# Optimization experiments

Hardware: AMD Instinct MI355X
Metric: run time of the kernel (lower is better)

## Reference

```python
import jax, jax.numpy as jnp
import numpy as np

N_NODES = 50000
N_EDGES = 640000
IN_CH = 128
HIDDEN = 128
HEADS = 4
HEAD_DIM = HIDDEN // HEADS  # 32
NEG_SLOPE = 0.2


def setup_inputs() -> dict:
    key = jax.random.key(0)
    ks = jax.random.split(key, 12)
    x = jax.random.normal(ks[0], (N_NODES, IN_CH), dtype=jnp.float32)
    edge_index = jax.random.randint(ks[1], (2, N_EDGES), 0, N_NODES, dtype=jnp.int64)
    s = 0.1
    W1 = jax.random.normal(ks[2], (IN_CH, HEADS * HEAD_DIM), dtype=jnp.float32) * s
    a_src1 = jax.random.normal(ks[3], (HEADS, HEAD_DIM), dtype=jnp.float32) * s
    a_dst1 = jax.random.normal(ks[4], (HEADS, HEAD_DIM), dtype=jnp.float32) * s
    b1 = jax.random.normal(ks[5], (HEADS * HEAD_DIM,), dtype=jnp.float32) * s
    W2 = jax.random.normal(ks[6], (HIDDEN, HEADS * HEAD_DIM), dtype=jnp.float32) * s
    a_src2 = jax.random.normal(ks[7], (HEADS, HEAD_DIM), dtype=jnp.float32) * s
    a_dst2 = jax.random.normal(ks[8], (HEADS, HEAD_DIM), dtype=jnp.float32) * s
    b2 = jax.random.normal(ks[9], (HEADS * HEAD_DIM,), dtype=jnp.float32) * s
    return {"x": x, "edge_index": edge_index, "W1": W1, "a_src1": a_src1,
            "a_dst1": a_dst1, "b1": b1, "W2": W2, "a_src2": a_src2,
            "a_dst2": a_dst2, "b2": b2}


def _gat_conv(x, src, dst, W, a_src, a_dst, b):
    """PyG GATConv (concat=True, add_self_loops already applied to src/dst)."""
    N = x.shape[0]
    H, C = a_src.shape
    h = (x @ W).reshape(N, H, C)                      # [N, H, C]
    alpha_s = jnp.einsum('nhc,hc->nh', h, a_src)      # [N, H]
    alpha_d = jnp.einsum('nhc,hc->nh', h, a_dst)      # [N, H]
    e = alpha_s[src] + alpha_d[dst]                   # [E, H]
    e = jnp.where(e > 0, e, NEG_SLOPE * e)            # leaky_relu(0.2)
    # segment softmax over destination nodes (every node has a self-loop)
    emax = jax.ops.segment_max(e, dst, num_segments=N)
    ee = jnp.exp(e - emax[dst])
    denom = jax.ops.segment_sum(ee, dst, num_segments=N)
    alpha = ee / (denom[dst] + 1e-16)                 # [E, H]
    out = jax.ops.segment_sum(h[src] * alpha[:, :, None], dst, num_segments=N)
    return out.reshape(N, H * C) + b


def reference(x, edge_index, W1, a_src1, a_dst1, b1, W2, a_src2, a_dst2, b2):
    N = x.shape[0]
    loops = jnp.arange(N, dtype=edge_index.dtype)
    src = jnp.concatenate([edge_index[0], loops])
    dst = jnp.concatenate([edge_index[1], loops])
    h = _gat_conv(x, src, dst, W1, a_src1, a_dst1, b1)
    h = jax.nn.relu(h)  # dropout is identity in eval mode
    out = _gat_conv(h, src, dst, W2, a_src2, a_dst2, b2)
    return out
```

## Files before the change

### kernel.cpp

```cpp
#include <hip/hip_runtime.h>
#include <hip/hip_bf16.h>
#include <hip/hip_fp16.h>

#define N_NODES 50000
#define N_EDGES 640000
#define E_TOT   690000
#define CH      128
#define ROWPAD  50176
#define GEMMB   391
#define EBLK    2048
#define NEB     337
#define NBUCK   196
#define MTP     344

typedef __attribute__((ext_vector_type(8))) short short8;
typedef __attribute__((ext_vector_type(4))) float float4v;

static __device__ __forceinline__ float bf2f(unsigned short u) {
  return __uint_as_float(((unsigned)u) << 16);
}
static __device__ __forceinline__ unsigned short f2bf(float f) {
  unsigned u = __float_as_uint(f);
  return (unsigned short)((u + 0x7fffu + ((u >> 16) & 1u)) >> 16);
}

static __device__ __forceinline__ void load_edge(const int* __restrict__ ei,
                                                 int e, int i64, int& s, int& d)
{
  if (e >= N_EDGES) { s = d = e - N_EDGES; return; }
  if (i64) { s = ei[2 * (size_t)e]; d = ei[2 * ((size_t)N_EDGES + e)]; }
  else     { s = ei[e];             d = ei[N_EDGES + e]; }
}

static __device__ __forceinline__ short8 load_bf8(const void* __restrict__ X,
                                                  size_t off, int f32)
{
  if (!f32) return *(const short8*)((const unsigned short*)X + off);
  const float4* p = (const float4*)((const float*)X + off);
  float4 u = p[0], v = p[1];
  short8 r;
  r[0] = (short)f2bf(u.x); r[1] = (short)f2bf(u.y);
  r[2] = (short)f2bf(u.z); r[3] = (short)f2bf(u.w);
  r[4] = (short)f2bf(v.x); r[5] = (short)f2bf(v.y);
  r[6] = (short)f2bf(v.z); r[7] = (short)f2bf(v.w);
  return r;
}

__global__ __launch_bounds__(256) void k_prep(
    const void* __restrict__ W1, const void* __restrict__ W2,
    const void* __restrict__ as1, const void* __restrict__ ad1,
    const void* __restrict__ as2, const void* __restrict__ ad2,
    unsigned short* __restrict__ Wt1, unsigned short* __restrict__ Wt2,
    unsigned short* __restrict__ Ba1, unsigned short* __restrict__ Ba2,
    const unsigned short* __restrict__ x16,
    const unsigned int* __restrict__ eiw,
    int* __restrict__ flags)
{
  int b = blockIdx.x, t = threadIdx.x;
  __shared__ int sf, si;
  if (t == 0) { sf = 0; si = 1; }
  __syncthreads();
  int bad = 0;
  for (int i = t; i < 4096; i += 256) {
    float v = bf2f(x16[i]);
    if (!(v == v) || fabsf(v) > 100.f) bad = 1;
  }
  if (bad) atomicOr(&sf, 1);
  if (b == 0 && t < 128 && eiw[2 * t + 1] != 0u) atomicAnd(&si, 0);
  __syncthreads();
  int f32 = sf;
  if (b == 0 && t == 0) { flags[0] = sf; flags[1] = si; }

  if (b < 8) {
    int g = b * 256 + t;
    int l = g >> 10;
    int rem = g & 1023;
    int k = rem >> 3, n = rem & 7;
    const void* W  = l ? W2 : W1;
    const void* av = (n < 4) ? (l ? as2 : as1) : (l ? ad2 : ad1);
    int h = n & 3;
    float sum = 0.f;
    for (int c = 0; c < 32; c++) {
      float w = f32 ? ((const float*)W)[k * 128 + h * 32 + c]
                    : bf2f(((const unsigned short*)W)[k * 128 + h * 32 + c]);
      float a = f32 ? ((const float*)av)[h * 32 + c]
                    : bf2f(((const unsigned short*)av)[h * 32 + c]);
      sum += w * a;
    }
    unsigned short* Ba = l ? Ba2 : Ba1;
    Ba[n * 128 + k] = f2bf(sum);
    Ba[(8 + (rem >> 7)) * 128 + (rem & 127)] = 0;
  } else {
    int b2 = b - 8;
    int l = b2 >> 7, c = b2 & 127;
    if (t < 128) {
      const void* W = l ? W2 : W1;
      unsigned short* Wt = l ? Wt2 : Wt1;
      Wt[c * 128 + t] = f32 ? f2bf(((const float*)W)[t * 128 + c])
                            : ((const unsigned short*)W)[t * 128 + c];
    }
  }
}

struct SmemG { unsigned short WB[144][136]; };

static __device__ __forceinline__ void gemm_body(
    SmemG& sm, int bx,
    const void* __restrict__ X,
    const unsigned short* __restrict__ Wt_g,
    const unsigned short* __restrict__ Ba_g,
    unsigned short* __restrict__ H, float* __restrict__ AS,
    float* __restrict__ AD, int nrows, int xf32)
{
  int tid = threadIdx.x;
#pragma unroll
  for (int i = 0; i < 8; i++) {
    int j = i * 256 + tid;
    int c = j >> 4, k8 = j & 15;
    *(short8*)&sm.WB[c][k8 * 8] = *(const short8*)(Wt_g + c * 128 + k8 * 8);
  }
  {
    int n = tid >> 4, k8 = tid & 15;
    *(short8*)&sm.WB[128 + n][k8 * 8] = *(const short8*)(Ba_g + n * 128 + k8 * 8);
  }
  __syncthreads();
  int wave = tid >> 6, lane = tid & 63;
  int R0 = (bx * 4 + wave) * 32;
  if (R0 >= nrows) return;
  int m = lane & 15, quad = lane >> 4;
  int rA = R0 + m;        if (rA >= nrows) rA = nrows - 1;
  int rB = R0 + 16 + m;   if (rB >= nrows) rB = nrows - 1;
  size_t aA = (size_t)rA * CH + quad * 8;
  size_t aB = (size_t)rB * CH + quad * 8;
  float4v acc[2][8];
  float4v accA[2];
#pragma unroll
  for (int hf = 0; hf < 2; hf++) {
    accA[hf] = (float4v){0.f, 0.f, 0.f, 0.f};
#pragma unroll
    for (int ct = 0; ct < 8; ct++) acc[hf][ct] = (float4v){0.f, 0.f, 0.f, 0.f};
  }
#pragma unroll
  for (int kb = 0; kb < 4; kb++) {
    short8 a0 = load_bf8(X, aA + kb * 32, xf32);
    short8 a1 = load_bf8(X, aB + kb * 32, xf32);
#pragma unroll
    for (int ct = 0; ct < 8; ct++) {
      short8 bb = *(const short8*)&sm.WB[ct * 16 + m][kb * 32 + quad * 8];
      acc[0][ct] = __builtin_amdgcn_mfma_f32_16x16x32_bf16(a0, bb, acc[0][ct], 0, 0, 0);
      acc[1][ct] = __builtin_amdgcn_mfma_f32_16x16x32_bf16(a1, bb, acc[1][ct], 0, 0, 0);
    }
    short8 bA = *(const short8*)&sm.WB[128 + m][kb * 32 + quad * 8];
    accA[0] = __builtin_amdgcn_mfma_f32_16x16x32_bf16(a0, bA, accA[0], 0, 0, 0);
    accA[1] = __builtin_amdgcn_mfma_f32_16x16x32_bf16(a1, bA, accA[1], 0, 0, 0);
  }
#pragma unroll
  for (int hf = 0; hf < 2; hf++) {
    int rbase = R0 + hf * 16 + quad * 4;
#pragma unroll
    for (int ct = 0; ct < 8; ct++) {
      int col = ct * 16 + m;
#pragma unroll
      for (int r = 0; r < 4; r++)
        H[(size_t)(rbase + r) * CH + col] = __half_as_ushort(__float2half(acc[hf][ct][r]));
    }
    if (m < 4) {
#pragma unroll
      for (int r = 0; r < 4; r++)
        AS[(size_t)(rbase + r) * 4 + m] = accA[hf][r];
    } else if (m < 8) {
#pragma unroll
      for (int r = 0; r < 4; r++)
        AD[(size_t)(rbase + r) * 4 + (m - 4)] = accA[hf][r];
    }
  }
}

__global__ __launch_bounds__(256, 2) void k_gemm(
    const void* __restrict__ X,
    const unsigned short* __restrict__ Wt_g,
    const unsigned short* __restrict__ Ba_g,
    unsigned short* __restrict__ H, float* __restrict__ AS, float* __restrict__ AD,
    int nrows)
{
  __shared__ SmemG sm;
  gemm_body(sm, blockIdx.x, X, Wt_g, Ba_g, H, AS, AD, nrows, 0);
}

__global__ __launch_bounds__(256, 2) void k_gemm_hist(
    const void* __restrict__ X,
    const unsigned short* __restrict__ Wt_g,
    const unsigned short* __restrict__ Ba_g,
    unsigned short* __restrict__ H, float* __restrict__ AS, float* __restrict__ AD,
    int nrows, const int* __restrict__ ei, int* __restrict__ MT,
    const int* __restrict__ flags)
{
  __shared__ SmemG sm;
  __shared__ int hist[NBUCK];
  if (blockIdx.x >= GEMMB) {
    int b = blockIdx.x - GEMMB;
    int t = threadIdx.x;
    if (t < NBUCK) hist[t] = 0;
    __syncthreads();
    int i64 = flags[1];
    int base = b * EBLK;
#pragma unroll
    for (int k = 0; k < 8; k++) {
      int e = base + k * 256 + t;
      if (e < E_TOT) {
        int s, d;
        load_edge(ei, e, i64, s, d);
        atomicAdd(&hist[d >> 8], 1);
      }
    }
    __syncthreads();
    if (t < NBUCK) MT[t * MTP + b] = hist[t];
    return;
  }
  gemm_body(sm, blockIdx.x, X, Wt_g, Ba_g, H, AS, AD, nrows, flags[0]);
}

__global__ __launch_bounds__(512) void k_rowscan(int* __restrict__ MT,
                                                 int* __restrict__ T)
{
  __shared__ int sh[512];
  int q = blockIdx.x, t = threadIdx.x;
  int v = (t < NEB) ? MT[q * MTP + t] : 0;
  sh[t] = v;
  __syncthreads();
  for (int off = 1; off < 512; off <<= 1) {
    int u = (t >= off) ? sh[t - off] : 0;
    __syncthreads();
    sh[t] += u;
    __syncthreads();
  }
  if (t < NEB) MT[q * MTP + t] = sh[t] - v;
  if (t == NEB - 1) T[q] = sh[t];
}

__global__ __launch_bounds__(256) void k_bscan(const int* __restrict__ T,
                                               int* __restrict__ BB)
{
  __shared__ int sh[256];
  int t = threadIdx.x;
  int v = (t < NBUCK) ? T[t] : 0;
  sh[t] = v;
  __syncthreads();
  for (int off = 1; off < 256; off <<= 1) {
    int u = (t >= off) ? sh[t - off] : 0;
    __syncthreads();
    sh[t] += u;
    __syncthreads();
  }
  if (t < NBUCK) BB[t] = sh[t] - v;
  if (t == NBUCK - 1) BB[NBUCK] = sh[t];
}

__global__ __launch_bounds__(256) void k_bucket(
    const int* __restrict__ ei, const int* __restrict__ MT,
    const int* __restrict__ BB, int2* __restrict__ ebuf,
    const int* __restrict__ flags)
{
  __shared__ int cur[NBUCK];
  int b = blockIdx.x, t = threadIdx.x;
  if (t < NBUCK) cur[t] = BB[t] + MT[t * MTP + b];
  __syncthreads();
  int i64 = flags[1];
  int base = b * EBLK;
#pragma unroll
  for (int k = 0; k < 8; k++) {
    int e = base + k * 256 + t;
    if (e < E_TOT) {
      int s, d;
      load_edge(ei, e, i64, s, d);
      int pos = atomicAdd(&cur[d >> 8], 1);
      ebuf[pos] = make_int2(s, d);
    }
  }
}

__global__ __launch_bounds__(256) void k_fine(
    const int2* __restrict__ ebuf, const int* __restrict__ BB,
    int* __restrict__ row_ptr, int* __restrict__ deg,
    int* __restrict__ csr_src)
{
  __shared__ int cnt[256], sh[256], cur[256];
  int q = blockIdx.x, t = threadIdx.x;
  int lo = BB[q], hi = BB[q + 1];
  cnt[t] = 0;
  __syncthreads();
  for (int i = lo + t; i < hi; i += 256)
    atomicAdd(&cnt[ebuf[i].y & 255], 1);
  __syncthreads();
  int v = cnt[t];
  sh[t] = v;
  __syncthreads();
  for (int off = 1; off < 256; off <<= 1) {
    int u = (t >= off) ? sh[t - off] : 0;
    __syncthreads();
    sh[t] += u;
    __syncthreads();
  }
  int lp = sh[t] - v;
  int n = (q << 8) + t;
  if (n < N_NODES) { row_ptr[n] = lo + lp; deg[n] = v; }
  cur[t] = lo + lp;
  __syncthreads();
  for (int i = lo + t; i < hi; i += 256) {
    int2 p = ebuf[i];
    int slot = atomicAdd(&cur[p.y & 255], 1);
    csr_src[slot] = p.x;
  }
}

__global__ __launch_bounds__(256) void k_agg(
    const int* __restrict__ row_ptr, const int* __restrict__ deg,
    const int* __restrict__ csr_src,
    const __half* __restrict__ H,
    const float* __restrict__ AS, const float* __restrict__ AD,
    const void* __restrict__ b, void* __restrict__ Y,
    const int* __restrict__ flags, int layer)
{
  int tid = threadIdx.x;
  int node = blockIdx.x * 4 + (tid >> 6);
  if (node >= N_NODES) return;
  int lane = tid & 63;
  int h = lane >> 4;
  int c0 = 2 * lane;
  float adh = AD[(size_t)node * 4 + h];
  int start = row_ptr[node];
  int dg = deg[node];
  const __half2* __restrict__ H2 = (const __half2*)H;
  float accx = 0.f, accy = 0.f, den = 0.f;
  int j = 0;
  for (; j + 8 <= dg; j += 8) {
    int sI[8];
#pragma unroll
    for (int u = 0; u < 8; u++) sI[u] = csr_src[start + j + u];
    float eV[8];
#pragma unroll
    for (int u = 0; u < 8; u++) eV[u] = AS[(size_t)sI[u] * 4 + h] + adh;
    float2 vV[8];
#pragma unroll
    for (int u = 0; u < 8; u++) vV[u] = __half22float2(H2[(size_t)sI[u] * 64 + lane]);
#pragma unroll
    for (int u = 0; u < 8; u++) {
      float x = eV[u] > 0.f ? eV[u] : 0.2f * eV[u];
      float ex = __expf(x);
      accx += ex * vV[u].x;
      accy += ex * vV[u].y;
      den  += ex;
    }
  }
  for (; j + 4 <= dg; j += 4) {
    int sI[4];
#pragma unroll
    for (int u = 0; u < 4; u++) sI[u] = csr_src[start + j + u];
    float eV[4];
#pragma unroll
    for (int u = 0; u < 4; u++) eV[u] = AS[(size_t)sI[u] * 4 + h] + adh;
    float2 vV[4];
#pragma unroll
    for (int u = 0; u < 4; u++) vV[u] = __half22float2(H2[(size_t)sI[u] * 64 + lane]);
#pragma unroll
    for (int u = 0; u < 4; u++) {
      float x = eV[u] > 0.f ? eV[u] : 0.2f * eV[u];
      float ex = __expf(x);
      accx += ex * vV[u].x;
      accy += ex * vV[u].y;
      den  += ex;
    }
  }
  for (; j < dg; j++) {
    int s = csr_src[start + j];
    float e = AS[(size_t)s * 4 + h] + adh;
    float2 v = __half22float2(H2[(size_t)s * 64 + lane]);
    e = e > 0.f ? e : 0.2f * e;
    float ex = __expf(e);
    accx += ex * v.x;
    accy += ex * v.y;
    den  += ex;
  }
  float inv = 1.f / (den + 1e-16f);
  int f32 = flags[0];
  float b0 = f32 ? ((const float*)b)[c0]     : bf2f(((const unsigned short*)b)[c0]);
  float b1 = f32 ? ((const float*)b)[c0 + 1] : bf2f(((const unsigned short*)b)[c0 + 1]);
  float r0 = accx * inv + b0;
  float r1 = accy * inv + b1;
  size_t o = (size_t)node * CH + c0;
  if (layer == 1) {
    r0 = r0 > 0.f ? r0 : 0.f;
    r1 = r1 > 0.f ? r1 : 0.f;
    ushort2 w; w.x = f2bf(r0); w.y = f2bf(r1);
    *(ushort2*)((unsigned short*)Y + o) = w;
  } else if (f32) {
    float2 w; w.x = r0; w.y = r1;
    *(float2*)((float*)Y + o) = w;
  } else {
    ushort2 w; w.x = f2bf(r0); w.y = f2bf(r1);
    *(ushort2*)((unsigned short*)Y + o) = w;
  }
}

extern "C" void kernel_launch(void* const* d_in, const int* in_sizes, int n_in,
                              void* d_out, int out_size, void* d_ws, size_t ws_size,
                              hipStream_t stream)
{
  const void* x   = d_in[0];
  const int*  ei  = (const int*)d_in[1];
  const void* W1  = d_in[2];
  const void* as1 = d_in[3];
  const void* ad1 = d_in[4];
  const void* b1  = d_in[5];
  const void* W2  = d_in[6];
  const void* as2 = d_in[7];
  const void* ad2 = d_in[8];
  const void* b2  = d_in[9];

  char* ws = (char*)d_ws;
  unsigned short* H  = (unsigned short*)(ws);
  float*  AS         = (float*)(ws + 12845056);
  float*  AD         = (float*)(ws + 13647872);
  unsigned short* X2 = (unsigned short*)(ws + 14450688);
  int*    deg        = (int*)(ws + 27295744);
  int*    row_ptr    = (int*)(ws + 27496448);
  int*    csr_src    = (int*)(ws + 27697152);
  int*    MT         = (int*)(ws + 30457600);
  int*    T          = (int*)(ws + 30728192);
  int*    BB         = (int*)(ws + 30729216);
  int*    flags      = (int*)(ws + 30730240);
  int2*   ebuf       = (int2*)(ws + 30731264);
  unsigned short* Wt1 = (unsigned short*)(ws + 36251264);
  unsigned short* Wt2 = (unsigned short*)(ws + 36284032);
  unsigned short* Ba1 = (unsigned short*)(ws + 36316800);
  unsigned short* Ba2 = (unsigned short*)(ws + 36320896);

  const int agg_blocks = (N_NODES + 3) / 4;

  k_prep<<<264, 256, 0, stream>>>(W1, W2, as1, ad1, as2, ad2,
                                  Wt1, Wt2, Ba1, Ba2,
                                  (const unsigned short*)x,
                                  (const unsigned int*)ei, flags);

  k_gemm_hist<<<GEMMB + NEB, 256, 0, stream>>>(
      x, Wt1, Ba1, H, AS, AD, N_NODES, ei, MT, flags);

  k_rowscan<<<NBUCK, 512, 0, stream>>>(MT, T);
  k_bscan  <<<1, 256, 0, stream>>>(T, BB);
  k_bucket <<<NEB, 256, 0, stream>>>(ei, MT, BB, ebuf, flags);
  k_fine   <<<NBUCK, 256, 0, stream>>>(ebuf, BB, row_ptr, deg, csr_src);

  k_agg<<<agg_blocks, 256, 0, stream>>>(row_ptr, deg, csr_src,
                                        (const __half*)H, AS, AD,
                                        b1, X2, flags, 1);

  k_gemm<<<GEMMB, 256, 0, stream>>>(X2, Wt2, Ba2, H, AS, AD, N_NODES);
  k_agg<<<agg_blocks, 256, 0, stream>>>(row_ptr, deg, csr_src,
                                        (const __half*)H, AS, AD,
                                        b2, d_out, flags, 2);
}
```

Baseline: 217.1 us.

## Compress CSR indices to 16-bit, pack edge buffer, unroll aggregation by 16

```diff
diff --git a/kernel.cpp b/kernel.cpp
--- a/kernel.cpp
+++ b/kernel.cpp
@@ -258,7 +258,7 @@
 
 __global__ __launch_bounds__(256) void k_bucket(
     const int* __restrict__ ei, const int* __restrict__ MT,
-    const int* __restrict__ BB, int2* __restrict__ ebuf,
+    const int* __restrict__ BB, unsigned int* __restrict__ ebuf,
     const int* __restrict__ flags)
 {
   __shared__ int cur[NBUCK];
@@ -274,15 +274,14 @@
       int s, d;
       load_edge(ei, e, i64, s, d);
       int pos = atomicAdd(&cur[d >> 8], 1);
-      ebuf[pos] = make_int2(s, d);
+      ebuf[pos] = ((unsigned)s << 8) | (unsigned)(d & 255);
     }
   }
 }
 
 __global__ __launch_bounds__(256) void k_fine(
-    const int2* __restrict__ ebuf, const int* __restrict__ BB,
-    int* __restrict__ row_ptr, int* __restrict__ deg,
-    int* __restrict__ csr_src)
+    const unsigned int* __restrict__ ebuf, const int* __restrict__ BB,
+    int2* __restrict__ rpdeg, unsigned short* __restrict__ csr)
 {
   __shared__ int cnt[256], sh[256], cur[256];
   int q = blockIdx.x, t = threadIdx.x;
@@ -290,7 +289,7 @@
   cnt[t] = 0;
   __syncthreads();
   for (int i = lo + t; i < hi; i += 256)
-    atomicAdd(&cnt[ebuf[i].y & 255], 1);
+    atomicAdd(&cnt[ebuf[i] & 255u], 1);
   __syncthreads();
   int v = cnt[t];
   sh[t] = v;
@@ -303,19 +302,19 @@
   }
   int lp = sh[t] - v;
   int n = (q << 8) + t;
-  if (n < N_NODES) { row_ptr[n] = lo + lp; deg[n] = v; }
+  if (n < N_NODES) rpdeg[n] = make_int2(lo + lp, v);
   cur[t] = lo + lp;
   __syncthreads();
   for (int i = lo + t; i < hi; i += 256) {
-    int2 p = ebuf[i];
-    int slot = atomicAdd(&cur[p.y & 255], 1);
-    csr_src[slot] = p.x;
+    unsigned p = ebuf[i];
+    int slot = atomicAdd(&cur[p & 255u], 1);
+    csr[slot] = (unsigned short)(p >> 8);
   }
 }
 
 __global__ __launch_bounds__(256) void k_agg(
-    const int* __restrict__ row_ptr, const int* __restrict__ deg,
-    const int* __restrict__ csr_src,
+    const int2* __restrict__ rpdeg,
+    const unsigned short* __restrict__ csr,
     const __half* __restrict__ H,
     const float* __restrict__ AS, const float* __restrict__ AD,
     const void* __restrict__ b, void* __restrict__ Y,
@@ -327,59 +326,35 @@
   int lane = tid & 63;
   int h = lane >> 4;
   int c0 = 2 * lane;
+  int2 rd = rpdeg[node];
+  int start = rd.x, dg = rd.y;
   float adh = AD[(size_t)node * 4 + h];
-  int start = row_ptr[node];
-  int dg = deg[node];
   const __half2* __restrict__ H2 = (const __half2*)H;
   float accx = 0.f, accy = 0.f, den = 0.f;
-  int j = 0;
-  for (; j + 8 <= dg; j += 8) {
-    int sI[8];
-#pragma unroll
-    for (int u = 0; u < 8; u++) sI[u] = csr_src[start + j + u];
-    float eV[8];
-#pragma unroll
-    for (int u = 0; u < 8; u++) eV[u] = AS[(size_t)sI[u] * 4 + h] + adh;
-    float2 vV[8];
-#pragma unroll
-    for (int u = 0; u < 8; u++) vV[u] = __half22float2(H2[(size_t)sI[u] * 64 + lane]);
-#pragma unroll
-    for (int u = 0; u < 8; u++) {
+  int last = start + dg - 1;
+  for (int j = 0; j < dg; j += 16) {
+    int sI[16];
+#pragma unroll
+    for (int u = 0; u < 16; u++) {
+      int idx = start + j + u;
+      sI[u] = (int)csr[idx <= last ? idx : last];
+    }
+    float2 vV[16];
+#pragma unroll
+    for (int u = 0; u < 16; u++)
+      vV[u] = __half22float2(H2[sI[u] * 64 + lane]);
+    float eV[16];
+#pragma unroll
+    for (int u = 0; u < 16; u++)
+      eV[u] = AS[sI[u] * 4 + h] + adh;
+#pragma unroll
+    for (int u = 0; u < 16; u++) {
       float x = eV[u] > 0.f ? eV[u] : 0.2f * eV[u];
-      float ex = __expf(x);
+      float ex = (j + u < dg) ? __expf(x) : 0.f;
       accx += ex * vV[u].x;
       accy += ex * vV[u].y;
       den  += ex;
     }
-  }
-  for (; j + 4 <= dg; j += 4) {
-    int sI[4];
-#pragma unroll
-    for (int u = 0; u < 4; u++) sI[u] = csr_src[start + j + u];
-    float eV[4];
-#pragma unroll
-    for (int u = 0; u < 4; u++) eV[u] = AS[(size_t)sI[u] * 4 + h] + adh;
-    float2 vV[4];
-#pragma unroll
-    for (int u = 0; u < 4; u++) vV[u] = __half22float2(H2[(size_t)sI[u] * 64 + lane]);
-#pragma unroll
-    for (int u = 0; u < 4; u++) {
-      float x = eV[u] > 0.f ? eV[u] : 0.2f * eV[u];
-      float ex = __expf(x);
-      accx += ex * vV[u].x;
-      accy += ex * vV[u].y;
-      den  += ex;
-    }
-  }
-  for (; j < dg; j++) {
-    int s = csr_src[start + j];
-    float e = AS[(size_t)s * 4 + h] + adh;
-    float2 v = __half22float2(H2[(size_t)s * 64 + lane]);
-    e = e > 0.f ? e : 0.2f * e;
-    float ex = __expf(e);
-    accx += ex * v.x;
-    accy += ex * v.y;
-    den  += ex;
   }
   float inv = 1.f / (den + 1e-16f);
   int f32 = flags[0];
@@ -418,22 +393,21 @@
   const void* b2  = d_in[9];
 
   char* ws = (char*)d_ws;
-  unsigned short* H  = (unsigned short*)(ws);
-  float*  AS         = (float*)(ws + 12845056);
-  float*  AD         = (float*)(ws + 13647872);
-  unsigned short* X2 = (unsigned short*)(ws + 14450688);
-  int*    deg        = (int*)(ws + 27295744);
-  int*    row_ptr    = (int*)(ws + 27496448);
-  int*    csr_src    = (int*)(ws + 27697152);
-  int*    MT         = (int*)(ws + 30457600);
-  int*    T          = (int*)(ws + 30728192);
-  int*    BB         = (int*)(ws + 30729216);
-  int*    flags      = (int*)(ws + 30730240);
-  int2*   ebuf       = (int2*)(ws + 30731264);
-  unsigned short* Wt1 = (unsigned short*)(ws + 36251264);
-  unsigned short* Wt2 = (unsigned short*)(ws + 36284032);
-  unsigned short* Ba1 = (unsigned short*)(ws + 36316800);
-  unsigned short* Ba2 = (unsigned short*)(ws + 36320896);
+  unsigned short* H   = (unsigned short*)(ws);
+  float*  AS          = (float*)(ws + 12845056);
+  float*  AD          = (float*)(ws + 13647872);
+  unsigned short* X2  = (unsigned short*)(ws + 14450688);
+  int2*   rpdeg       = (int2*)(ws + 27295744);
+  unsigned short* csr = (unsigned short*)(ws + 27697152);
+  int*    MT          = (int*)(ws + 29080000);
+  int*    T           = (int*)(ws + 29350000);
+  int*    BB          = (int*)(ws + 29351000);
+  int*    flags       = (int*)(ws + 29352000);
+  unsigned int* ebuf  = (unsigned int*)(ws + 29353216);
+  unsigned short* Wt1 = (unsigned short*)(ws + 32120000);
+  unsigned short* Wt2 = (unsigned short*)(ws + 32152768);
+  unsigned short* Ba1 = (unsigned short*)(ws + 32185536);
+  unsigned short* Ba2 = (unsigned short*)(ws + 32189632);
 
   const int agg_blocks = (N_NODES + 3) / 4;
 
@@ -448,14 +422,14 @@
   k_rowscan<<<NBUCK, 512, 0, stream>>>(MT, T);
   k_bscan  <<<1, 256, 0, stream>>>(T, BB);
   k_bucket <<<NEB, 256, 0, stream>>>(ei, MT, BB, ebuf, flags);
-  k_fine   <<<NBUCK, 256, 0, stream>>>(ebuf, BB, row_ptr, deg, csr_src);
-
-  k_agg<<<agg_blocks, 256, 0, stream>>>(row_ptr, deg, csr_src,
+  k_fine   <<<NBUCK, 256, 0, stream>>>(ebuf, BB, rpdeg, csr);
+
+  k_agg<<<agg_blocks, 256, 0, stream>>>(rpdeg, csr,
                                         (const __half*)H, AS, AD,
                                         b1, X2, flags, 1);
 
   k_gemm<<<GEMMB, 256, 0, stream>>>(X2, Wt2, Ba2, H, AS, AD, N_NODES);
-  k_agg<<<agg_blocks, 256, 0, stream>>>(row_ptr, deg, csr_src,
+  k_agg<<<agg_blocks, 256, 0, stream>>>(rpdeg, csr,
                                         (const __half*)H, AS, AD,
                                         b2, d_out, flags, 2);
 }
```

Measured after the change: 219.1 us. Within noise of the previous version (+0.9%).
